# Kernel tuning notes

Hardware: AMD Instinct MI355X
Metric: run time of the kernel (lower is better)

## Reference

```python
import jax, jax.numpy as jnp
import numpy as np
from jax import lax

WIN = 11
SIGMA = 1.5
C1 = 0.01 ** 2
C2 = 0.03 ** 2


def _gauss_window(c):
    x = np.arange(WIN) - WIN // 2
    g = np.exp(-(x ** 2) / (2.0 * SIGMA ** 2))
    g = g / g.sum()
    w2d = np.outer(g, g).astype(np.float32)  # [11,11]
    return jnp.asarray(np.broadcast_to(w2d, (c, 1, WIN, WIN)).copy())


def _dwconv(x, kernel, groups):
    # x: [B,C,H,W], kernel: [C,1,kh,kw] depthwise, stride 1, SAME padding
    return lax.conv_general_dilated(
        x, kernel, window_strides=(1, 1), padding='SAME',
        dimension_numbers=('NCHW', 'OIHW', 'NCHW'),
        feature_group_count=groups)


_SOBEL_X = jnp.asarray(np.array([[-1, 0, 1], [-2, 0, 2], [-1, 0, 1]], np.float32))
_SOBEL_Y = jnp.asarray(np.array([[1, 2, 1], [0, 0, 0], [-1, -2, -1]], np.float32))


def _sobel_xy(x):
    # x: [B,3,H,W] -> depthwise 3x3 sobel on each channel (same as per-channel conv2d)
    c = x.shape[1]
    kx = jnp.broadcast_to(_SOBEL_X, (c, 1, 3, 3))
    ky = jnp.broadcast_to(_SOBEL_Y, (c, 1, 3, 3))
    return _dwconv(x, kx, c), _dwconv(x, ky, c)


def _rgb2ycrcb(im):
    R, G, B = im[:, 0:1], im[:, 1:2], im[:, 2:3]
    Y = 0.299 * R + 0.587 * G + 0.114 * B
    Cr = (R - Y) * 0.713 + 0.5
    Cb = (B - Y) * 0.564 + 0.5
    return Y, Cr, Cb


def _ssim(img1, img2, channel):
    w = _gauss_window(channel)
    mu1 = _dwconv(img1, w, channel)
    mu2 = _dwconv(img2, w, channel)
    mu1_sq = mu1 * mu1
    mu2_sq = mu2 * mu2
    mu12 = mu1 * mu2
    s1 = _dwconv(img1 * img1, w, channel) - mu1_sq
    s2 = _dwconv(img2 * img2, w, channel) - mu2_sq
    s12 = _dwconv(img1 * img2, w, channel) - mu12
    ssim_map = ((2 * mu12 + C1) * (2 * s12 + C2)) / ((mu1_sq + mu2_sq + C1) * (s1 + s2 + C2))
    return ssim_map.mean()


def _l1(a, b):
    return jnp.mean(jnp.abs(a - b))


def setup_inputs() -> dict:
    key = jax.random.key(0)
    k1, k2, k3 = jax.random.split(key, 3)
    shp = (16, 3, 512, 512)
    return {
        'input_vis': jax.random.uniform(k1, shp, jnp.float32),
        'input_ir': jax.random.uniform(k2, shp, jnp.float32),
        'fuse': jax.random.uniform(k3, shp, jnp.float32),
    }


def reference(input_vis, input_ir, fuse):
    # color components
    _, Cr_F, Cb_F = _rgb2ycrcb(fuse)
    _, Cr_V, Cb_V = _rgb2ycrcb(input_vis)
    Y_ir = input_ir[:, 0:1]

    # sobel gradients (depthwise over 3 channels == per-channel conv + cat)
    Fgx, Fgy = _sobel_xy(fuse)
    Vgx, Vgy = _sobel_xy(input_vis)
    Igx, Igy = _sobel_xy(input_ir)
    joint_gx = jnp.maximum(Vgx, Igx)
    joint_gy = jnp.maximum(Vgy, Igy)
    joint_int = jnp.maximum(input_vis, input_ir)

    con_loss = _l1(fuse, joint_int)
    gradient_loss = 0.5 * _l1(Fgx, joint_gx) + 0.5 * _l1(Fgy, joint_gy)
    color_loss = _l1(Cb_F, Cb_V) + _l1(Cr_F, Cr_V)

    # SSIM: rgb-vs-fused (3ch) and ir-Y vs gray(fused) (1ch)
    ssim_rgb = _ssim(input_vis, fuse, 3)
    gray_fused = (0.2989 * fuse[:, 0:1] + 0.587 * fuse[:, 1:2] + 0.114 * fuse[:, 2:3])
    ssim_ir = _ssim(Y_ir, gray_fused, 1)
    ssim_loss = 1.0 - (ssim_rgb + ssim_ir) / 2.0

    return 0.5 * con_loss + 0.2 * gradient_loss + 1.0 * color_loss + 0.1 * ssim_loss
```

## Files before the change

### kernel.cpp

```cpp
#include <hip/hip_runtime.h>

#define IMG_H 512
#define IMG_W 512
#define CH_STRIDE (IMG_H*IMG_W)
#define IMG_STRIDE (3*CH_STRIDE)

using f4    = __attribute__((ext_vector_type(4))) float;
using h4    = __attribute__((ext_vector_type(4))) _Float16;
using h8    = __attribute__((ext_vector_type(8))) _Float16;
using f32x4 = __attribute__((ext_vector_type(4))) float;

#define NSLOT 64
#define SLOT_F 32

__global__ __launch_bounds__(256) void k_zero(float* __restrict__ acc) {
  int i = threadIdx.x;
  *(f4*)&acc[i*8]     = f4{0,0,0,0};
  *(f4*)&acc[i*8 + 4] = f4{0,0,0,0};
}

__device__ __forceinline__ float block_sum(float v, float* red) {
  #pragma unroll
  for (int o = 32; o > 0; o >>= 1) v += __shfl_down(v, o, 64);
  __syncthreads();
  if ((threadIdx.x & 63) == 0) red[threadIdx.x >> 6] = v;
  __syncthreads();
  return red[0] + red[1] + red[2] + red[3];
}

#define R1W 68
#define R1N (18*R1W)

#define SXW 88
#define SXH 26
#define SF_STRIDE (SXH*SXW)
#define HB_OFF    (4*SF_STRIDE)
#define HB_F      (64*32)
#define WH_OFF    (HB_OFF + 4*HB_F)
#define WV_OFF    (WH_OFF + 512)
#define SMEM_H    (WV_OFF + 512)
#define SMEM_BYTES (SMEM_H*2)

#define N_SSIM 16384

__global__ __launch_bounds__(256, 4) void k_main(
    const float* __restrict__ vis, const float* __restrict__ ir,
    const float* __restrict__ fuse, float* __restrict__ acc)
{
  __shared__ __align__(16) char smem[SMEM_BYTES];
  __shared__ float red[4];
  const int tid = threadIdx.x;
  const int bid = blockIdx.x;
  float* aslot = acc + (bid & (NSLOT-1))*SLOT_F;

  if (bid < N_SSIM) {
    const int z = bid >> 8;
    const int n = z >> 2, pair = z & 3;
    const int x0 = (bid & 7)*64;
    const int y0 = ((bid >> 3) & 31)*16;
    _Float16* S = (_Float16*)smem;

    for (int i = tid; i < 1024; i += 256) {
      int m = i & 511;
      int col = m >> 5, k = m & 31;
      int j = (i < 512) ? (k - col - 3) : (k - col);
      float w = 0.f;
      if ((unsigned)j < 11u) {
        float d = (float)(j - 5);
        w = exp2f(-d*d*0.32059889798f) * 0.26601255681f;
      }
      S[(i < 512 ? WH_OFF : WV_OFF) + m] = (_Float16)w;
    }

    if (pair < 3) {
      const float* xb = vis  + (n*3 + pair)*CH_STRIDE;
      const float* yb = fuse + (n*3 + pair)*CH_STRIDE;
      for (int i = tid; i < SXH*20; i += 256) {
        int row = i / 20, k = i - row*20;
        int gy = y0 - 5 + row, gx = x0 - 8 + 4*k;
        f4 xv = {0,0,0,0}, yv = {0,0,0,0};
        if ((unsigned)gy < IMG_H && (unsigned)gx < IMG_W) {
          int off = gy*IMG_W + gx;
          xv = *(const f4*)&xb[off];
          yv = *(const f4*)&yb[off];
        }
        int ib = row*SXW + 4*k;
        h4 ax, by, pp, qq;
        #pragma unroll
        for (int j = 0; j < 4; ++j) {
          float xa = xv[j], ya = yv[j];
          ax[j] = (_Float16)xa;
          by[j] = (_Float16)ya;
          pp[j] = (_Float16)(xa*xa + ya*ya);
          qq[j] = (_Float16)(xa*ya);
        }
        *(h4*)&S[0*SF_STRIDE + ib] = ax;
        *(h4*)&S[1*SF_STRIDE + ib] = by;
        *(h4*)&S[2*SF_STRIDE + ib] = pp;
        *(h4*)&S[3*SF_STRIDE + ib] = qq;
      }
    } else {
      const float* xb = ir   + n*IMG_STRIDE;
      const float* fb = fuse + n*IMG_STRIDE;
      for (int i = tid; i < SXH*20; i += 256) {
        int row = i / 20, k = i - row*20;
        int gy = y0 - 5 + row, gx = x0 - 8 + 4*k;
        f4 xv = {0,0,0,0}, yv = {0,0,0,0};
        if ((unsigned)gy < IMG_H && (unsigned)gx < IMG_W) {
          int off = gy*IMG_W + gx;
          xv = *(const f4*)&xb[off];
          f4 rr = *(const f4*)&fb[off];
          f4 gg = *(const f4*)&fb[off + CH_STRIDE];
          f4 bb = *(const f4*)&fb[off + 2*CH_STRIDE];
          #pragma unroll
          for (int j = 0; j < 4; ++j)
            yv[j] = 0.2989f*rr[j] + 0.587f*gg[j] + 0.114f*bb[j];
        }
        int ib = row*SXW + 4*k;
        h4 ax, by, pp, qq;
        #pragma unroll
        for (int j = 0; j < 4; ++j) {
          float xa = xv[j], ya = yv[j];
          ax[j] = (_Float16)xa;
          by[j] = (_Float16)ya;
          pp[j] = (_Float16)(xa*xa + ya*ya);
          qq[j] = (_Float16)(xa*ya);
        }
        *(h4*)&S[0*SF_STRIDE + ib] = ax;
        *(h4*)&S[1*SF_STRIDE + ib] = by;
        *(h4*)&S[2*SF_STRIDE + ib] = pp;
        *(h4*)&S[3*SF_STRIDE + ib] = qq;
      }
    }
    __syncthreads();

    const int lr = tid & 15;
    const int lg = (tid >> 4) & 3;
    const int wv = tid >> 6;

    {
      h8 bh = *(const h8*)&S[WH_OFF + lr*32 + lg*8];
      const int xo = wv*16;
      #pragma unroll
      for (int rt = 0; rt < 2; ++rt) {
        int row_s = rt*16 + lr;
        int rcl = row_s > 25 ? 25 : row_s;
        bool zz = row_s > 25;
        #pragma unroll
        for (int f = 0; f < 4; ++f) {
          h8 a = *(const h8*)&S[f*SF_STRIDE + rcl*SXW + xo + lg*8];
          if (zz) a = h8{(_Float16)0,(_Float16)0,(_Float16)0,(_Float16)0,
                         (_Float16)0,(_Float16)0,(_Float16)0,(_Float16)0};
          f32x4 d = __builtin_amdgcn_mfma_f32_16x16x32_f16(
                        a, bh, f32x4{0.f,0.f,0.f,0.f}, 0, 0, 0);
          int px = xo + lr;
          int k0 = rt*16 + lg*4;
          h4 hv;
          #pragma unroll
          for (int r = 0; r < 4; ++r) hv[r] = (_Float16)d[r];
          int sgrp = (px ^ (px >> 2)) & 3;
          int b = k0 << 1;
          int sb = ((((b >> 4) ^ sgrp) << 4) | (b & 15));
          *(h4*)&S[HB_OFF + f*HB_F + px*32 + (sb >> 1)] = hv;
        }
      }
    }
    __syncthreads();

    float ss = 0.f;
    {
      h8 bv = *(const h8*)&S[WV_OFF + lr*32 + lg*8];
      const int pxA = wv*16 + lr;
      const int sgrp = (pxA ^ (pxA >> 2)) & 3;
      f32x4 dd[4];
      #pragma unroll
      for (int f = 0; f < 4; ++f) {
        int gi = lg ^ sgrp;
        h8 a = *(const h8*)&S[HB_OFF + f*HB_F + pxA*32 + gi*8];
        dd[f] = __builtin_amdgcn_mfma_f32_16x16x32_f16(
                    a, bv, f32x4{0.f,0.f,0.f,0.f}, 0, 0, 0);
      }
      #pragma unroll
      for (int r = 0; r < 4; ++r) {
        float mu1 = dd[0][r], mu2 = dd[1][r];
        float sP  = dd[2][r], sQ  = dd[3][r];
        float mu12 = mu1*mu2, mss = mu1*mu1 + mu2*mu2;
        float s12 = sQ - mu12, sps = sP - mss;
        ss += ((2.f*mu12 + 1e-4f)*(2.f*s12 + 9e-4f)) /
              ((mss + 1e-4f)*(sps + 9e-4f));
      }
    }
    float tot = block_sum(ss, red);
    if (tid == 0) atomicAdd(&aslot[(pair == 3) ? 6 : 5], tot);

  } else {
    const int r = bid - N_SSIM;
    const int x0 = (r & 7)*64;
    const int y0 = ((r >> 3) & 31)*16;
    const int n  = r >> 8;
    float* s = (float*)smem;
    const int ox = (tid & 15)*4;
    const int oy = tid >> 4;

    float con=0.f, gxs=0.f, gys=0.f, cbs=0.f, crs=0.f;
    float pv[3][4], pf[3][4];

    for (int c = 0; c < 3; ++c) {
      const float* pv0 = vis  + (n*3 + c)*CH_STRIDE;
      const float* pi0 = ir   + (n*3 + c)*CH_STRIDE;
      const float* pf0 = fuse + (n*3 + c)*CH_STRIDE;
      for (int i = tid; i < 864; i += 256) {
        int f = i / 288;
        int rr = i - f*288;
        int row = rr >> 4, k = rr & 15;
        int gy = y0 - 1 + row, gx = x0 + 4*k;
        f4 v = {0,0,0,0};
        const float* bp = (f == 0) ? pv0 : ((f == 1) ? pi0 : pf0);
        if ((unsigned)gy < IMG_H) v = *(const f4*)&bp[gy*IMG_W + gx];
        float* dst = s + f*R1N + row*R1W + 1 + 4*k;
        dst[0]=v.x; dst[1]=v.y; dst[2]=v.z; dst[3]=v.w;
      }
      if (tid < 108) {
        int f = tid / 36;
        int rr = tid - f*36;
        int row = rr >> 1, side = rr & 1;
        int gy = y0 - 1 + row;
        int gx = side ? (x0 + 64) : (x0 - 1);
        float v = 0.f;
        const float* bp = (f == 0) ? pv0 : ((f == 1) ? pi0 : pf0);
        if ((unsigned)gx < IMG_W && (unsigned)gy < IMG_H) v = bp[gy*IMG_W + gx];
        s[f*R1N + row*R1W + (side ? 65 : 0)] = v;
      }
      __syncthreads();

      float cen[3][4], gxv[3][4], gyv[3][4];
      #pragma unroll
      for (int t = 0; t < 3; ++t) {
        const float* sf = s + t*R1N;
        float r0[8], r1[8], r2[8];
        {
          f4 a = *(const f4*)&sf[(oy+0)*R1W + ox], b = *(const f4*)&sf[(oy+0)*R1W + ox + 4];
          r0[0]=a.x; r0[1]=a.y; r0[2]=a.z; r0[3]=a.w; r0[4]=b.x; r0[5]=b.y; r0[6]=b.z; r0[7]=b.w;
        }
        {
          f4 a = *(const f4*)&sf[(oy+1)*R1W + ox], b = *(const f4*)&sf[(oy+1)*R1W + ox + 4];
          r1[0]=a.x; r1[1]=a.y; r1[2]=a.z; r1[3]=a.w; r1[4]=b.x; r1[5]=b.y; r1[6]=b.z; r1[7]=b.w;
        }
        {
          f4 a = *(const f4*)&sf[(oy+2)*R1W + ox], b = *(const f4*)&sf[(oy+2)*R1W + ox + 4];
          r2[0]=a.x; r2[1]=a.y; r2[2]=a.z; r2[3]=a.w; r2[4]=b.x; r2[5]=b.y; r2[6]=b.z; r2[7]=b.w;
        }
        #pragma unroll
        for (int j = 0; j < 4; ++j) {
          gxv[t][j] = (r0[j+2]-r0[j]) + 2.f*(r1[j+2]-r1[j]) + (r2[j+2]-r2[j]);
          gyv[t][j] = (r0[j] + 2.f*r0[j+1] + r0[j+2]) - (r2[j] + 2.f*r2[j+1] + r2[j+2]);
          cen[t][j] = r1[j+1];
        }
      }
      #pragma unroll
      for (int j = 0; j < 4; ++j) {
        con += fabsf(cen[2][j] - fmaxf(cen[0][j], cen[1][j]));
        gxs += fabsf(gxv[2][j] - fmaxf(gxv[0][j], gxv[1][j]));
        gys += fabsf(gyv[2][j] - fmaxf(gyv[0][j], gyv[1][j]));
        pv[c][j] = cen[0][j];
        pf[c][j] = cen[2][j];
      }
      __syncthreads();
    }

    #pragma unroll
    for (int j = 0; j < 4; ++j) {
      float Yf = 0.299f*pf[0][j] + 0.587f*pf[1][j] + 0.114f*pf[2][j];
      float Yv = 0.299f*pv[0][j] + 0.587f*pv[1][j] + 0.114f*pv[2][j];
      crs += fabsf(0.713f*((pf[0][j]-Yf) - (pv[0][j]-Yv)));
      cbs += fabsf(0.564f*((pf[2][j]-Yf) - (pv[2][j]-Yv)));
    }

    float r0 = block_sum(con, red);
    float r1 = block_sum(gxs, red);
    float r2 = block_sum(gys, red);
    float r3 = block_sum(cbs, red);
    float r4 = block_sum(crs, red);
    if (tid == 0) {
      atomicAdd(&aslot[0], r0);
      atomicAdd(&aslot[1], r1);
      atomicAdd(&aslot[2], r2);
      atomicAdd(&aslot[3], r3);
      atomicAdd(&aslot[4], r4);
    }
  }
}

__global__ __launch_bounds__(64) void k_final(
    const float* __restrict__ acc, float* __restrict__ out)
{
  int lane = threadIdx.x;
  float s[7];
  #pragma unroll
  for (int c = 0; c < 7; ++c) {
    float x = acc[lane*SLOT_F + c];
    #pragma unroll
    for (int o = 32; o > 0; o >>= 1) x += __shfl_down(x, o, 64);
    s[c] = x;
  }
  if (lane == 0) {
    const float N3 = 16.f*3.f*512.f*512.f;
    const float N1 = 16.f*512.f*512.f;
    float con_loss  = s[0] / N3;
    float grad_loss = 0.5f*(s[1]/N3) + 0.5f*(s[2]/N3);
    float color_loss = s[3]/N1 + s[4]/N1;
    float ssim_loss = 1.f - (s[5]/N3 + s[6]/N1)*0.5f;
    out[0] = 0.5f*con_loss + 0.2f*grad_loss + color_loss + 0.1f*ssim_loss;
  }
}

extern "C" void kernel_launch(void* const* d_in, const int* in_sizes, int n_in,
                              void* d_out, int out_size, void* d_ws, size_t ws_size,
                              hipStream_t stream) {
  (void)in_sizes; (void)n_in; (void)out_size; (void)ws_size;
  const float* vis  = (const float*)d_in[0];
  const float* ir   = (const float*)d_in[1];
  const float* fuse = (const float*)d_in[2];
  float* out = (float*)d_out;
  float* acc = (float*)d_ws;

  k_zero<<<dim3(1,1,1), dim3(256,1,1), 0, stream>>>(acc);
  k_main<<<dim3(20480,1,1), dim3(256,1,1), 0, stream>>>(vis, ir, fuse, acc);
  k_final<<<dim3(1,1,1), dim3(64,1,1), 0, stream>>>(acc, out);
}
```

Measured before the change: 253.6 us.

## Shrink SSIM LDS footprint, compute weights in registers, interleave block types

The SSIM path now stores only the two fp16 input planes in LDS and forms the squared and cross products in registers before the horizontal MFMA. Gaussian weights are built directly in registers instead of staged through shared memory. This cuts LDS use so the launch bound can rise to 6 blocks per CU. The Sobel/L1 blocks are interleaved with the SSIM blocks (one per five) and read global memory directly instead of through LDS, with per-wave atomics replacing block reductions. In exchange there are more global loads and atomics, and the squares are now computed from fp16-rounded inputs, which changes precision.

After: 556.7 us. 120% more time.

```diff
diff --git a/kernel.cpp b/kernel.cpp
--- a/kernel.cpp
+++ b/kernel.cpp
@@ -19,57 +19,65 @@
   *(f4*)&acc[i*8 + 4] = f4{0,0,0,0};
 }
 
-__device__ __forceinline__ float block_sum(float v, float* red) {
-  #pragma unroll
-  for (int o = 32; o > 0; o >>= 1) v += __shfl_down(v, o, 64);
-  __syncthreads();
-  if ((threadIdx.x & 63) == 0) red[threadIdx.x >> 6] = v;
-  __syncthreads();
-  return red[0] + red[1] + red[2] + red[3];
-}
-
-#define R1W 68
-#define R1N (18*R1W)
-
-#define SXW 88
+__device__ __forceinline__ h4 cvt4(f4 v) {
+  return h4{(_Float16)v.x,(_Float16)v.y,(_Float16)v.z,(_Float16)v.w};
+}
+__device__ __forceinline__ h8 zero8() {
+  return h8{(_Float16)0,(_Float16)0,(_Float16)0,(_Float16)0,
+            (_Float16)0,(_Float16)0,(_Float16)0,(_Float16)0};
+}
+
+#define SXW 80
 #define SXH 26
 #define SF_STRIDE (SXH*SXW)
-#define HB_OFF    (4*SF_STRIDE)
+#define HB_OFF    (2*SF_STRIDE)
 #define HB_F      (64*32)
-#define WH_OFF    (HB_OFF + 4*HB_F)
-#define WV_OFF    (WH_OFF + 512)
-#define SMEM_H    (WV_OFF + 512)
-#define SMEM_BYTES (SMEM_H*2)
-
-#define N_SSIM 16384
-
-__global__ __launch_bounds__(256, 4) void k_main(
+#define SMEM_H    (HB_OFF + 4*HB_F)
+#define SMEM_BYTES (SMEM_H*2 + 128)
+
+__global__ __launch_bounds__(256, 6) void k_main(
     const float* __restrict__ vis, const float* __restrict__ ir,
     const float* __restrict__ fuse, float* __restrict__ acc)
 {
   __shared__ __align__(16) char smem[SMEM_BYTES];
-  __shared__ float red[4];
+  float* red = (float*)(smem + SMEM_H*2);
   const int tid = threadIdx.x;
   const int bid = blockIdx.x;
   float* aslot = acc + (bid & (NSLOT-1))*SLOT_F;
 
-  if (bid < N_SSIM) {
-    const int z = bid >> 8;
+  const int sb = bid / 5;
+  const int rm = bid - sb*5;
+
+  if (rm < 4) {
+    const int si = sb*4 + rm;
+    const int z = si >> 8;
     const int n = z >> 2, pair = z & 3;
-    const int x0 = (bid & 7)*64;
-    const int y0 = ((bid >> 3) & 31)*16;
+    const int x0 = (si & 7)*64;
+    const int y0 = ((si >> 3) & 31)*16;
     _Float16* S = (_Float16*)smem;
 
-    for (int i = tid; i < 1024; i += 256) {
-      int m = i & 511;
-      int col = m >> 5, k = m & 31;
-      int j = (i < 512) ? (k - col - 3) : (k - col);
-      float w = 0.f;
-      if ((unsigned)j < 11u) {
-        float d = (float)(j - 5);
-        w = exp2f(-d*d*0.32059889798f) * 0.26601255681f;
-      }
-      S[(i < 512 ? WH_OFF : WV_OFF) + m] = (_Float16)w;
+    const int lr = tid & 15;
+    const int lg = (tid >> 4) & 3;
+    const int wvw = tid >> 6;
+    const int xo = wvw*16;
+
+    h8 bh, bv;
+    #pragma unroll
+    for (int e = 0; e < 8; ++e) {
+      int k = lg*8 + e;
+      int jh = k - lr - 3;
+      int jv = k - lr;
+      float wh = 0.f, wvv = 0.f;
+      if ((unsigned)jh < 11u) {
+        float d = (float)(jh - 5);
+        wh = exp2f(-d*d*0.32059889798f) * 0.26601255681f;
+      }
+      if ((unsigned)jv < 11u) {
+        float d = (float)(jv - 5);
+        wvv = exp2f(-d*d*0.32059889798f) * 0.26601255681f;
+      }
+      bh[e] = (_Float16)wh;
+      bv[e] = (_Float16)wvv;
     }
 
     if (pair < 3) {
@@ -85,19 +93,8 @@
           yv = *(const f4*)&yb[off];
         }
         int ib = row*SXW + 4*k;
-        h4 ax, by, pp, qq;
-        #pragma unroll
-        for (int j = 0; j < 4; ++j) {
-          float xa = xv[j], ya = yv[j];
-          ax[j] = (_Float16)xa;
-          by[j] = (_Float16)ya;
-          pp[j] = (_Float16)(xa*xa + ya*ya);
-          qq[j] = (_Float16)(xa*ya);
-        }
-        *(h4*)&S[0*SF_STRIDE + ib] = ax;
-        *(h4*)&S[1*SF_STRIDE + ib] = by;
-        *(h4*)&S[2*SF_STRIDE + ib] = pp;
-        *(h4*)&S[3*SF_STRIDE + ib] = qq;
+        *(h4*)&S[ib]             = cvt4(xv);
+        *(h4*)&S[SF_STRIDE + ib] = cvt4(yv);
       }
     } else {
       const float* xb = ir   + n*IMG_STRIDE;
@@ -117,177 +114,168 @@
             yv[j] = 0.2989f*rr[j] + 0.587f*gg[j] + 0.114f*bb[j];
         }
         int ib = row*SXW + 4*k;
-        h4 ax, by, pp, qq;
-        #pragma unroll
-        for (int j = 0; j < 4; ++j) {
-          float xa = xv[j], ya = yv[j];
-          ax[j] = (_Float16)xa;
-          by[j] = (_Float16)ya;
-          pp[j] = (_Float16)(xa*xa + ya*ya);
-          qq[j] = (_Float16)(xa*ya);
-        }
-        *(h4*)&S[0*SF_STRIDE + ib] = ax;
-        *(h4*)&S[1*SF_STRIDE + ib] = by;
-        *(h4*)&S[2*SF_STRIDE + ib] = pp;
-        *(h4*)&S[3*SF_STRIDE + ib] = qq;
+        *(h4*)&S[ib]             = cvt4(xv);
+        *(h4*)&S[SF_STRIDE + ib] = cvt4(yv);
       }
     }
     __syncthreads();
 
-    const int lr = tid & 15;
-    const int lg = (tid >> 4) & 3;
-    const int wv = tid >> 6;
-
     {
-      h8 bh = *(const h8*)&S[WH_OFF + lr*32 + lg*8];
-      const int xo = wv*16;
+      const int px = xo + lr;
+      const int sgrp = (px ^ (px >> 2)) & 3;
       #pragma unroll
       for (int rt = 0; rt < 2; ++rt) {
         int row_s = rt*16 + lr;
         int rcl = row_s > 25 ? 25 : row_s;
-        bool zz = row_s > 25;
+        int rbase = rcl*SXW + xo + lg*8;
+        h8 a = *(const h8*)&S[rbase];
+        h8 b = *(const h8*)&S[SF_STRIDE + rbase];
+        if (row_s > 25) { a = zero8(); b = zero8(); }
+        h8 p = a*a + b*b;
+        h8 q = a*b;
+        f32x4 d0 = __builtin_amdgcn_mfma_f32_16x16x32_f16(
+                       a, bh, f32x4{0.f,0.f,0.f,0.f}, 0, 0, 0);
+        f32x4 d1 = __builtin_amdgcn_mfma_f32_16x16x32_f16(
+                       b, bh, f32x4{0.f,0.f,0.f,0.f}, 0, 0, 0);
+        f32x4 d2 = __builtin_amdgcn_mfma_f32_16x16x32_f16(
+                       p, bh, f32x4{0.f,0.f,0.f,0.f}, 0, 0, 0);
+        f32x4 d3 = __builtin_amdgcn_mfma_f32_16x16x32_f16(
+                       q, bh, f32x4{0.f,0.f,0.f,0.f}, 0, 0, 0);
+        int k0 = rt*16 + lg*4;
+        int bb2 = k0 << 1;
+        int sbk = ((((bb2 >> 4) ^ sgrp) << 4) | (bb2 & 15));
+        int base = HB_OFF + px*32 + (sbk >> 1);
+        h4 h0, h1, h2c, h3;
         #pragma unroll
-        for (int f = 0; f < 4; ++f) {
-          h8 a = *(const h8*)&S[f*SF_STRIDE + rcl*SXW + xo + lg*8];
-          if (zz) a = h8{(_Float16)0,(_Float16)0,(_Float16)0,(_Float16)0,
-                         (_Float16)0,(_Float16)0,(_Float16)0,(_Float16)0};
-          f32x4 d = __builtin_amdgcn_mfma_f32_16x16x32_f16(
-                        a, bh, f32x4{0.f,0.f,0.f,0.f}, 0, 0, 0);
-          int px = xo + lr;
-          int k0 = rt*16 + lg*4;
-          h4 hv;
-          #pragma unroll
-          for (int r = 0; r < 4; ++r) hv[r] = (_Float16)d[r];
-          int sgrp = (px ^ (px >> 2)) & 3;
-          int b = k0 << 1;
-          int sb = ((((b >> 4) ^ sgrp) << 4) | (b & 15));
-          *(h4*)&S[HB_OFF + f*HB_F + px*32 + (sb >> 1)] = hv;
-        }
+        for (int r2 = 0; r2 < 4; ++r2) {
+          h0[r2] = (_Float16)d0[r2];
+          h1[r2] = (_Float16)d1[r2];
+          h2c[r2] = (_Float16)d2[r2];
+          h3[r2] = (_Float16)d3[r2];
+        }
+        *(h4*)&S[base + 0*HB_F] = h0;
+        *(h4*)&S[base + 1*HB_F] = h1;
+        *(h4*)&S[base + 2*HB_F] = h2c;
+        *(h4*)&S[base + 3*HB_F] = h3;
       }
     }
     __syncthreads();
 
     float ss = 0.f;
     {
-      h8 bv = *(const h8*)&S[WV_OFF + lr*32 + lg*8];
-      const int pxA = wv*16 + lr;
+      const int pxA = xo + lr;
       const int sgrp = (pxA ^ (pxA >> 2)) & 3;
+      const int gi = lg ^ sgrp;
       f32x4 dd[4];
       #pragma unroll
       for (int f = 0; f < 4; ++f) {
-        int gi = lg ^ sgrp;
         h8 a = *(const h8*)&S[HB_OFF + f*HB_F + pxA*32 + gi*8];
         dd[f] = __builtin_amdgcn_mfma_f32_16x16x32_f16(
                     a, bv, f32x4{0.f,0.f,0.f,0.f}, 0, 0, 0);
       }
       #pragma unroll
-      for (int r = 0; r < 4; ++r) {
-        float mu1 = dd[0][r], mu2 = dd[1][r];
-        float sP  = dd[2][r], sQ  = dd[3][r];
+      for (int r2 = 0; r2 < 4; ++r2) {
+        float mu1 = dd[0][r2], mu2 = dd[1][r2];
+        float sP  = dd[2][r2], sQ  = dd[3][r2];
         float mu12 = mu1*mu2, mss = mu1*mu1 + mu2*mu2;
         float s12 = sQ - mu12, sps = sP - mss;
         ss += ((2.f*mu12 + 1e-4f)*(2.f*s12 + 9e-4f)) /
               ((mss + 1e-4f)*(sps + 9e-4f));
       }
     }
-    float tot = block_sum(ss, red);
-    if (tid == 0) atomicAdd(&aslot[(pair == 3) ? 6 : 5], tot);
+    #pragma unroll
+    for (int o = 32; o > 0; o >>= 1) ss += __shfl_down(ss, o, 64);
+    if ((tid & 63) == 0) atomicAdd(&aslot[(pair == 3) ? 6 : 5], ss);
 
   } else {
-    const int r = bid - N_SSIM;
+    const int r = sb;
     const int x0 = (r & 7)*64;
     const int y0 = ((r >> 3) & 31)*16;
     const int n  = r >> 8;
-    float* s = (float*)smem;
-    const int ox = (tid & 15)*4;
-    const int oy = tid >> 4;
+    const int gx = x0 + 4*(tid & 15);
+    const int gy = y0 + (tid >> 4);
 
     float con=0.f, gxs=0.f, gys=0.f, cbs=0.f, crs=0.f;
-    float pv[3][4], pf[3][4];
+    float pv0[4], pv2[4], pf0[4], pf2[4], Yv[4], Yf[4];
+    #pragma unroll
+    for (int j = 0; j < 4; ++j) { Yv[j]=0.f; Yf[j]=0.f; }
 
     for (int c = 0; c < 3; ++c) {
-      const float* pv0 = vis  + (n*3 + c)*CH_STRIDE;
-      const float* pi0 = ir   + (n*3 + c)*CH_STRIDE;
-      const float* pf0 = fuse + (n*3 + c)*CH_STRIDE;
-      for (int i = tid; i < 864; i += 256) {
-        int f = i / 288;
-        int rr = i - f*288;
-        int row = rr >> 4, k = rr & 15;
-        int gy = y0 - 1 + row, gx = x0 + 4*k;
-        f4 v = {0,0,0,0};
-        const float* bp = (f == 0) ? pv0 : ((f == 1) ? pi0 : pf0);
-        if ((unsigned)gy < IMG_H) v = *(const f4*)&bp[gy*IMG_W + gx];
-        float* dst = s + f*R1N + row*R1W + 1 + 4*k;
-        dst[0]=v.x; dst[1]=v.y; dst[2]=v.z; dst[3]=v.w;
-      }
-      if (tid < 108) {
-        int f = tid / 36;
-        int rr = tid - f*36;
-        int row = rr >> 1, side = rr & 1;
-        int gy = y0 - 1 + row;
-        int gx = side ? (x0 + 64) : (x0 - 1);
-        float v = 0.f;
-        const float* bp = (f == 0) ? pv0 : ((f == 1) ? pi0 : pf0);
-        if ((unsigned)gx < IMG_W && (unsigned)gy < IMG_H) v = bp[gy*IMG_W + gx];
-        s[f*R1N + row*R1W + (side ? 65 : 0)] = v;
-      }
-      __syncthreads();
-
-      float cen[3][4], gxv[3][4], gyv[3][4];
+      const float* bv_ = vis  + (n*3 + c)*CH_STRIDE;
+      const float* bi_ = ir   + (n*3 + c)*CH_STRIDE;
+      const float* bf_ = fuse + (n*3 + c)*CH_STRIDE;
+      const float yc = (c == 0) ? 0.299f : ((c == 1) ? 0.587f : 0.114f);
+      float mc[4], mx[4], my[4];
       #pragma unroll
       for (int t = 0; t < 3; ++t) {
-        const float* sf = s + t*R1N;
-        float r0[8], r1[8], r2[8];
-        {
-          f4 a = *(const f4*)&sf[(oy+0)*R1W + ox], b = *(const f4*)&sf[(oy+0)*R1W + ox + 4];
-          r0[0]=a.x; r0[1]=a.y; r0[2]=a.z; r0[3]=a.w; r0[4]=b.x; r0[5]=b.y; r0[6]=b.z; r0[7]=b.w;
-        }
-        {
-          f4 a = *(const f4*)&sf[(oy+1)*R1W + ox], b = *(const f4*)&sf[(oy+1)*R1W + ox + 4];
-          r1[0]=a.x; r1[1]=a.y; r1[2]=a.z; r1[3]=a.w; r1[4]=b.x; r1[5]=b.y; r1[6]=b.z; r1[7]=b.w;
-        }
-        {
-          f4 a = *(const f4*)&sf[(oy+2)*R1W + ox], b = *(const f4*)&sf[(oy+2)*R1W + ox + 4];
-          r2[0]=a.x; r2[1]=a.y; r2[2]=a.z; r2[3]=a.w; r2[4]=b.x; r2[5]=b.y; r2[6]=b.z; r2[7]=b.w;
-        }
+        const float* bp = (t == 0) ? bv_ : ((t == 1) ? bi_ : bf_);
+        float w[3][6];
+        #pragma unroll
+        for (int rr = 0; rr < 3; ++rr) {
+          int ry = gy - 1 + rr;
+          f4 m = {0,0,0,0}; float lft = 0.f, rgt = 0.f;
+          if ((unsigned)ry < IMG_H) {
+            const float* rp = bp + ry*IMG_W;
+            m = *(const f4*)&rp[gx];
+            if (gx > 0)   lft = rp[gx-1];
+            if (gx < 508) rgt = rp[gx+4];
+          }
+          w[rr][0]=lft; w[rr][1]=m.x; w[rr][2]=m.y; w[rr][3]=m.z;
+          w[rr][4]=m.w; w[rr][5]=rgt;
+        }
+        float cen[4], gxv[4], gyv[4];
         #pragma unroll
         for (int j = 0; j < 4; ++j) {
-          gxv[t][j] = (r0[j+2]-r0[j]) + 2.f*(r1[j+2]-r1[j]) + (r2[j+2]-r2[j]);
-          gyv[t][j] = (r0[j] + 2.f*r0[j+1] + r0[j+2]) - (r2[j] + 2.f*r2[j+1] + r2[j+2]);
-          cen[t][j] = r1[j+1];
-        }
-      }
-      #pragma unroll
-      for (int j = 0; j < 4; ++j) {
-        con += fabsf(cen[2][j] - fmaxf(cen[0][j], cen[1][j]));
-        gxs += fabsf(gxv[2][j] - fmaxf(gxv[0][j], gxv[1][j]));
-        gys += fabsf(gyv[2][j] - fmaxf(gyv[0][j], gyv[1][j]));
-        pv[c][j] = cen[0][j];
-        pf[c][j] = cen[2][j];
-      }
-      __syncthreads();
-    }
-
+          gxv[j] = (w[0][j+2]-w[0][j]) + 2.f*(w[1][j+2]-w[1][j]) + (w[2][j+2]-w[2][j]);
+          gyv[j] = (w[0][j] + 2.f*w[0][j+1] + w[0][j+2])
+                 - (w[2][j] + 2.f*w[2][j+1] + w[2][j+2]);
+          cen[j] = w[1][j+1];
+        }
+        if (t == 0) {
+          #pragma unroll
+          for (int j = 0; j < 4; ++j) {
+            mc[j]=cen[j]; mx[j]=gxv[j]; my[j]=gyv[j];
+            Yv[j] += yc*cen[j];
+            if (c == 0) pv0[j] = cen[j];
+            if (c == 2) pv2[j] = cen[j];
+          }
+        } else if (t == 1) {
+          #pragma unroll
+          for (int j = 0; j < 4; ++j) {
+            mc[j]=fmaxf(mc[j],cen[j]); mx[j]=fmaxf(mx[j],gxv[j]);
+            my[j]=fmaxf(my[j],gyv[j]);
+          }
+        } else {
+          #pragma unroll
+          for (int j = 0; j < 4; ++j) {
+            con += fabsf(cen[j] - mc[j]);
+            gxs += fabsf(gxv[j] - mx[j]);
+            gys += fabsf(gyv[j] - my[j]);
+            Yf[j] += yc*cen[j];
+            if (c == 0) pf0[j] = cen[j];
+            if (c == 2) pf2[j] = cen[j];
+          }
+        }
+      }
+    }
     #pragma unroll
     for (int j = 0; j < 4; ++j) {
-      float Yf = 0.299f*pf[0][j] + 0.587f*pf[1][j] + 0.114f*pf[2][j];
-      float Yv = 0.299f*pv[0][j] + 0.587f*pv[1][j] + 0.114f*pv[2][j];
-      crs += fabsf(0.713f*((pf[0][j]-Yf) - (pv[0][j]-Yv)));
-      cbs += fabsf(0.564f*((pf[2][j]-Yf) - (pv[2][j]-Yv)));
-    }
-
-    float r0 = block_sum(con, red);
-    float r1 = block_sum(gxs, red);
-    float r2 = block_sum(gys, red);
-    float r3 = block_sum(cbs, red);
-    float r4 = block_sum(crs, red);
-    if (tid == 0) {
-      atomicAdd(&aslot[0], r0);
-      atomicAdd(&aslot[1], r1);
-      atomicAdd(&aslot[2], r2);
-      atomicAdd(&aslot[3], r3);
-      atomicAdd(&aslot[4], r4);
-    }
+      crs += fabsf(0.713f*((pf0[j]-Yf[j]) - (pv0[j]-Yv[j])));
+      cbs += fabsf(0.564f*((pf2[j]-Yf[j]) - (pv2[j]-Yv[j])));
+    }
+
+    float sums[5] = {con, gxs, gys, cbs, crs};
+    const int lane = tid & 63, wvw = tid >> 6;
+    #pragma unroll
+    for (int i = 0; i < 5; ++i) {
+      float v = sums[i];
+      #pragma unroll
+      for (int o = 32; o > 0; o >>= 1) v += __shfl_down(v, o, 64);
+      if (lane == 0) red[wvw*5 + i] = v;
+    }
+    __syncthreads();
+    if (tid < 5)
+      atomicAdd(&aslot[tid], red[tid] + red[5+tid] + red[10+tid] + red[15+tid]);
   }
 }
 
```

## Process two SSIM row tiles per block with prefetch and on-the-fly products

Applied to the files above, without the earlier changes.

Each SSIM block now handles two 16-row tiles. Global loads for the second tile are issued before the first tile's horizontal MFMA pass and written to shared memory afterwards, so load latency overlaps compute. The squared and cross-product planes are formed in registers from the two staged fp16 inputs instead of being stored, which halves staging LDS. Gaussian weights are built in registers rather than shared memory, and the block reduction becomes per-wave atomics. The trade-offs are more registers, more atomics and fewer blocks, and squares are now taken of fp16-rounded inputs, which changes precision slightly.

Measured after the change: 236.1 us. 1.07x faster.

```diff
diff --git a/kernel.cpp b/kernel.cpp
--- a/kernel.cpp
+++ b/kernel.cpp
@@ -28,56 +28,153 @@
   return red[0] + red[1] + red[2] + red[3];
 }
 
+__device__ __forceinline__ h4 cvt4(f4 v) {
+  return h4{(_Float16)v.x,(_Float16)v.y,(_Float16)v.z,(_Float16)v.w};
+}
+__device__ __forceinline__ h8 zero8() {
+  return h8{(_Float16)0,(_Float16)0,(_Float16)0,(_Float16)0,
+            (_Float16)0,(_Float16)0,(_Float16)0,(_Float16)0};
+}
+
 #define R1W 68
 #define R1N (18*R1W)
 
 #define SXW 88
 #define SXH 26
 #define SF_STRIDE (SXH*SXW)
-#define HB_OFF    (4*SF_STRIDE)
+#define HB_OFF    (2*SF_STRIDE)
 #define HB_F      (64*32)
-#define WH_OFF    (HB_OFF + 4*HB_F)
-#define WV_OFF    (WH_OFF + 512)
-#define SMEM_H    (WV_OFF + 512)
-#define SMEM_BYTES (SMEM_H*2)
-
-#define N_SSIM 16384
+#define SMEM_H    (HB_OFF + 4*HB_F)
+#define SMEM_BYTES (SMEM_H*2 + 128)
+
+#define N_SSIM 8192
+
+__device__ __forceinline__ void phaseB(_Float16* S, h8 bh,
+                                       int lr, int lg, int xo) {
+  const int px = xo + lr;
+  const int sgrp = (px ^ (px >> 2)) & 3;
+  #pragma unroll
+  for (int rt = 0; rt < 2; ++rt) {
+    int row_s = rt*16 + lr;
+    int rcl = row_s > 25 ? 25 : row_s;
+    int rbase = rcl*SXW + xo + lg*8;
+    h8 a = *(const h8*)&S[rbase];
+    h8 b = *(const h8*)&S[SF_STRIDE + rbase];
+    if (row_s > 25) { a = zero8(); b = zero8(); }
+    h8 p = a*a + b*b;
+    h8 q = a*b;
+    f32x4 d0 = __builtin_amdgcn_mfma_f32_16x16x32_f16(
+                   a, bh, f32x4{0.f,0.f,0.f,0.f}, 0, 0, 0);
+    f32x4 d1 = __builtin_amdgcn_mfma_f32_16x16x32_f16(
+                   b, bh, f32x4{0.f,0.f,0.f,0.f}, 0, 0, 0);
+    f32x4 d2 = __builtin_amdgcn_mfma_f32_16x16x32_f16(
+                   p, bh, f32x4{0.f,0.f,0.f,0.f}, 0, 0, 0);
+    f32x4 d3 = __builtin_amdgcn_mfma_f32_16x16x32_f16(
+                   q, bh, f32x4{0.f,0.f,0.f,0.f}, 0, 0, 0);
+    int k0 = rt*16 + lg*4;
+    int bb2 = k0 << 1;
+    int sbk = ((((bb2 >> 4) ^ sgrp) << 4) | (bb2 & 15));
+    int base = HB_OFF + px*32 + (sbk >> 1);
+    h4 h0, h1, h2c, h3;
+    #pragma unroll
+    for (int r2 = 0; r2 < 4; ++r2) {
+      h0[r2]  = (_Float16)d0[r2];
+      h1[r2]  = (_Float16)d1[r2];
+      h2c[r2] = (_Float16)d2[r2];
+      h3[r2]  = (_Float16)d3[r2];
+    }
+    *(h4*)&S[base + 0*HB_F] = h0;
+    *(h4*)&S[base + 1*HB_F] = h1;
+    *(h4*)&S[base + 2*HB_F] = h2c;
+    *(h4*)&S[base + 3*HB_F] = h3;
+  }
+}
+
+__device__ __forceinline__ float phaseC(const _Float16* S, h8 bv,
+                                        int lr, int lg, int xo) {
+  const int pxA = xo + lr;
+  const int sgrp = (pxA ^ (pxA >> 2)) & 3;
+  const int gi = lg ^ sgrp;
+  f32x4 dd[4];
+  #pragma unroll
+  for (int f = 0; f < 4; ++f) {
+    h8 a = *(const h8*)&S[HB_OFF + f*HB_F + pxA*32 + gi*8];
+    dd[f] = __builtin_amdgcn_mfma_f32_16x16x32_f16(
+                a, bv, f32x4{0.f,0.f,0.f,0.f}, 0, 0, 0);
+  }
+  float ss = 0.f;
+  #pragma unroll
+  for (int r2 = 0; r2 < 4; ++r2) {
+    float mu1 = dd[0][r2], mu2 = dd[1][r2];
+    float sP  = dd[2][r2], sQ  = dd[3][r2];
+    float mu12 = mu1*mu2, mss = mu1*mu1 + mu2*mu2;
+    float s12 = sQ - mu12, sps = sP - mss;
+    ss += ((2.f*mu12 + 1e-4f)*(2.f*s12 + 9e-4f)) /
+          ((mss + 1e-4f)*(sps + 9e-4f));
+  }
+  return ss;
+}
 
 __global__ __launch_bounds__(256, 4) void k_main(
     const float* __restrict__ vis, const float* __restrict__ ir,
     const float* __restrict__ fuse, float* __restrict__ acc)
 {
   __shared__ __align__(16) char smem[SMEM_BYTES];
-  __shared__ float red[4];
+  float* red = (float*)(smem + SMEM_H*2);
   const int tid = threadIdx.x;
   const int bid = blockIdx.x;
   float* aslot = acc + (bid & (NSLOT-1))*SLOT_F;
 
   if (bid < N_SSIM) {
-    const int z = bid >> 8;
+    const int z = bid >> 7;
     const int n = z >> 2, pair = z & 3;
     const int x0 = (bid & 7)*64;
-    const int y0 = ((bid >> 3) & 31)*16;
+    const int y0a = ((bid >> 3) & 15)*32;
+    const int y0b = y0a + 16;
     _Float16* S = (_Float16*)smem;
 
-    for (int i = tid; i < 1024; i += 256) {
-      int m = i & 511;
-      int col = m >> 5, k = m & 31;
-      int j = (i < 512) ? (k - col - 3) : (k - col);
-      float w = 0.f;
-      if ((unsigned)j < 11u) {
-        float d = (float)(j - 5);
-        w = exp2f(-d*d*0.32059889798f) * 0.26601255681f;
-      }
-      S[(i < 512 ? WH_OFF : WV_OFF) + m] = (_Float16)w;
-    }
-
+    const int lr = tid & 15;
+    const int lg = (tid >> 4) & 3;
+    const int wvw = tid >> 6;
+    const int xo = wvw*16;
+
+    const float* xb;
+    const float* yb;
     if (pair < 3) {
-      const float* xb = vis  + (n*3 + pair)*CH_STRIDE;
-      const float* yb = fuse + (n*3 + pair)*CH_STRIDE;
+      xb = vis  + (n*3 + pair)*CH_STRIDE;
+      yb = fuse + (n*3 + pair)*CH_STRIDE;
+    } else {
+      xb = ir   + n*IMG_STRIDE;
+      yb = fuse + n*IMG_STRIDE;
+    }
+
+    h8 bh, bv;
+    #pragma unroll
+    for (int e = 0; e < 8; ++e) {
+      int k = lg*8 + e;
+      int jh = k - lr - 3;
+      int jv = k - lr;
+      float wh = 0.f, wvv = 0.f;
+      if ((unsigned)jh < 11u) {
+        float d = (float)(jh - 5);
+        wh = exp2f(-d*d*0.32059889798f) * 0.26601255681f;
+      }
+      if ((unsigned)jv < 11u) {
+        float d = (float)(jv - 5);
+        wvv = exp2f(-d*d*0.32059889798f) * 0.26601255681f;
+      }
+      bh[e] = (_Float16)wh;
+      bv[e] = (_Float16)wvv;
+    }
+
+    const int row0 = tid / 20,        k0c = tid - row0*20;
+    const int i1r  = tid + 256;
+    const int row1 = i1r / 20,        k1c = i1r - row1*20;
+
+    if (pair < 3) {
       for (int i = tid; i < SXH*20; i += 256) {
         int row = i / 20, k = i - row*20;
-        int gy = y0 - 5 + row, gx = x0 - 8 + 4*k;
+        int gy = y0a - 5 + row, gx = x0 - 8 + 4*k;
         f4 xv = {0,0,0,0}, yv = {0,0,0,0};
         if ((unsigned)gy < IMG_H && (unsigned)gx < IMG_W) {
           int off = gy*IMG_W + gx;
@@ -85,113 +182,113 @@
           yv = *(const f4*)&yb[off];
         }
         int ib = row*SXW + 4*k;
-        h4 ax, by, pp, qq;
-        #pragma unroll
-        for (int j = 0; j < 4; ++j) {
-          float xa = xv[j], ya = yv[j];
-          ax[j] = (_Float16)xa;
-          by[j] = (_Float16)ya;
-          pp[j] = (_Float16)(xa*xa + ya*ya);
-          qq[j] = (_Float16)(xa*ya);
-        }
-        *(h4*)&S[0*SF_STRIDE + ib] = ax;
-        *(h4*)&S[1*SF_STRIDE + ib] = by;
-        *(h4*)&S[2*SF_STRIDE + ib] = pp;
-        *(h4*)&S[3*SF_STRIDE + ib] = qq;
+        *(h4*)&S[ib]             = cvt4(xv);
+        *(h4*)&S[SF_STRIDE + ib] = cvt4(yv);
       }
     } else {
-      const float* xb = ir   + n*IMG_STRIDE;
-      const float* fb = fuse + n*IMG_STRIDE;
       for (int i = tid; i < SXH*20; i += 256) {
         int row = i / 20, k = i - row*20;
-        int gy = y0 - 5 + row, gx = x0 - 8 + 4*k;
+        int gy = y0a - 5 + row, gx = x0 - 8 + 4*k;
         f4 xv = {0,0,0,0}, yv = {0,0,0,0};
         if ((unsigned)gy < IMG_H && (unsigned)gx < IMG_W) {
           int off = gy*IMG_W + gx;
           xv = *(const f4*)&xb[off];
-          f4 rr = *(const f4*)&fb[off];
-          f4 gg = *(const f4*)&fb[off + CH_STRIDE];
-          f4 bb = *(const f4*)&fb[off + 2*CH_STRIDE];
+          f4 rr = *(const f4*)&yb[off];
+          f4 gg = *(const f4*)&yb[off + CH_STRIDE];
+          f4 bb = *(const f4*)&yb[off + 2*CH_STRIDE];
           #pragma unroll
           for (int j = 0; j < 4; ++j)
             yv[j] = 0.2989f*rr[j] + 0.587f*gg[j] + 0.114f*bb[j];
         }
         int ib = row*SXW + 4*k;
-        h4 ax, by, pp, qq;
+        *(h4*)&S[ib]             = cvt4(xv);
+        *(h4*)&S[SF_STRIDE + ib] = cvt4(yv);
+      }
+    }
+    __syncthreads();
+
+    f4 p0x = {0,0,0,0}, p0y = {0,0,0,0}, p1x = {0,0,0,0}, p1y = {0,0,0,0};
+    f4 q0g = {0,0,0,0}, q0b = {0,0,0,0}, q1g = {0,0,0,0}, q1b = {0,0,0,0};
+    {
+      int gy0 = y0b - 5 + row0, gx0 = x0 - 8 + 4*k0c;
+      int gy1 = y0b - 5 + row1, gx1 = x0 - 8 + 4*k1c;
+      bool v0 = (unsigned)gy0 < IMG_H && (unsigned)gx0 < IMG_W;
+      bool v1 = (unsigned)gy1 < IMG_H && (unsigned)gx1 < IMG_W;
+      int o0 = gy0*IMG_W + gx0, o1 = gy1*IMG_W + gx1;
+      if (pair < 3) {
+        if (v0) { p0x = *(const f4*)&xb[o0]; p0y = *(const f4*)&yb[o0]; }
+        if (v1) { p1x = *(const f4*)&xb[o1]; p1y = *(const f4*)&yb[o1]; }
+      } else {
+        if (v0) {
+          p0x = *(const f4*)&xb[o0];
+          p0y = *(const f4*)&yb[o0];
+          q0g = *(const f4*)&yb[o0 + CH_STRIDE];
+          q0b = *(const f4*)&yb[o0 + 2*CH_STRIDE];
+        }
+        if (v1) {
+          p1x = *(const f4*)&xb[o1];
+          p1y = *(const f4*)&yb[o1];
+          q1g = *(const f4*)&yb[o1 + CH_STRIDE];
+          q1b = *(const f4*)&yb[o1 + 2*CH_STRIDE];
+        }
+      }
+    }
+
+    phaseB(S, bh, lr, lg, xo);
+    __syncthreads();
+
+    {
+      int ib0 = row0*SXW + 4*k0c;
+      int ib1 = row1*SXW + 4*k1c;
+      if (pair < 3) {
+        *(h4*)&S[ib0]             = cvt4(p0x);
+        *(h4*)&S[SF_STRIDE + ib0] = cvt4(p0y);
+        *(h4*)&S[ib1]             = cvt4(p1x);
+        *(h4*)&S[SF_STRIDE + ib1] = cvt4(p1y);
+      } else {
+        f4 l0, l1;
         #pragma unroll
         for (int j = 0; j < 4; ++j) {
-          float xa = xv[j], ya = yv[j];
-          ax[j] = (_Float16)xa;
-          by[j] = (_Float16)ya;
-          pp[j] = (_Float16)(xa*xa + ya*ya);
-          qq[j] = (_Float16)(xa*ya);
-        }
-        *(h4*)&S[0*SF_STRIDE + ib] = ax;
-        *(h4*)&S[1*SF_STRIDE + ib] = by;
-        *(h4*)&S[2*SF_STRIDE + ib] = pp;
-        *(h4*)&S[3*SF_STRIDE + ib] = qq;
-      }
-    }
+          l0[j] = 0.2989f*p0y[j] + 0.587f*q0g[j] + 0.114f*q0b[j];
+          l1[j] = 0.2989f*p1y[j] + 0.587f*q1g[j] + 0.114f*q1b[j];
+        }
+        *(h4*)&S[ib0]             = cvt4(p0x);
+        *(h4*)&S[SF_STRIDE + ib0] = cvt4(l0);
+        *(h4*)&S[ib1]             = cvt4(p1x);
+        *(h4*)&S[SF_STRIDE + ib1] = cvt4(l1);
+      }
+      if (tid < 8) {
+        int k2 = tid + 12;
+        int gy2 = y0b + 20, gx2 = x0 - 8 + 4*k2;
+        f4 xv = {0,0,0,0}, yv = {0,0,0,0};
+        if ((unsigned)gy2 < IMG_H && (unsigned)gx2 < IMG_W) {
+          int off = gy2*IMG_W + gx2;
+          xv = *(const f4*)&xb[off];
+          if (pair < 3) yv = *(const f4*)&yb[off];
+          else {
+            f4 rr = *(const f4*)&yb[off];
+            f4 gg = *(const f4*)&yb[off + CH_STRIDE];
+            f4 bb = *(const f4*)&yb[off + 2*CH_STRIDE];
+            #pragma unroll
+            for (int j = 0; j < 4; ++j)
+              yv[j] = 0.2989f*rr[j] + 0.587f*gg[j] + 0.114f*bb[j];
+          }
+        }
+        int ib2 = 25*SXW + 4*k2;
+        *(h4*)&S[ib2]             = cvt4(xv);
+        *(h4*)&S[SF_STRIDE + ib2] = cvt4(yv);
+      }
+    }
+
+    float ss = phaseC(S, bv, lr, lg, xo);
     __syncthreads();
-
-    const int lr = tid & 15;
-    const int lg = (tid >> 4) & 3;
-    const int wv = tid >> 6;
-
-    {
-      h8 bh = *(const h8*)&S[WH_OFF + lr*32 + lg*8];
-      const int xo = wv*16;
-      #pragma unroll
-      for (int rt = 0; rt < 2; ++rt) {
-        int row_s = rt*16 + lr;
-        int rcl = row_s > 25 ? 25 : row_s;
-        bool zz = row_s > 25;
-        #pragma unroll
-        for (int f = 0; f < 4; ++f) {
-          h8 a = *(const h8*)&S[f*SF_STRIDE + rcl*SXW + xo + lg*8];
-          if (zz) a = h8{(_Float16)0,(_Float16)0,(_Float16)0,(_Float16)0,
-                         (_Float16)0,(_Float16)0,(_Float16)0,(_Float16)0};
-          f32x4 d = __builtin_amdgcn_mfma_f32_16x16x32_f16(
-                        a, bh, f32x4{0.f,0.f,0.f,0.f}, 0, 0, 0);
-          int px = xo + lr;
-          int k0 = rt*16 + lg*4;
-          h4 hv;
-          #pragma unroll
-          for (int r = 0; r < 4; ++r) hv[r] = (_Float16)d[r];
-          int sgrp = (px ^ (px >> 2)) & 3;
-          int b = k0 << 1;
-          int sb = ((((b >> 4) ^ sgrp) << 4) | (b & 15));
-          *(h4*)&S[HB_OFF + f*HB_F + px*32 + (sb >> 1)] = hv;
-        }
-      }
-    }
+    phaseB(S, bh, lr, lg, xo);
     __syncthreads();
-
-    float ss = 0.f;
-    {
-      h8 bv = *(const h8*)&S[WV_OFF + lr*32 + lg*8];
-      const int pxA = wv*16 + lr;
-      const int sgrp = (pxA ^ (pxA >> 2)) & 3;
-      f32x4 dd[4];
-      #pragma unroll
-      for (int f = 0; f < 4; ++f) {
-        int gi = lg ^ sgrp;
-        h8 a = *(const h8*)&S[HB_OFF + f*HB_F + pxA*32 + gi*8];
-        dd[f] = __builtin_amdgcn_mfma_f32_16x16x32_f16(
-                    a, bv, f32x4{0.f,0.f,0.f,0.f}, 0, 0, 0);
-      }
-      #pragma unroll
-      for (int r = 0; r < 4; ++r) {
-        float mu1 = dd[0][r], mu2 = dd[1][r];
-        float sP  = dd[2][r], sQ  = dd[3][r];
-        float mu12 = mu1*mu2, mss = mu1*mu1 + mu2*mu2;
-        float s12 = sQ - mu12, sps = sP - mss;
-        ss += ((2.f*mu12 + 1e-4f)*(2.f*s12 + 9e-4f)) /
-              ((mss + 1e-4f)*(sps + 9e-4f));
-      }
-    }
-    float tot = block_sum(ss, red);
-    if (tid == 0) atomicAdd(&aslot[(pair == 3) ? 6 : 5], tot);
+    ss += phaseC(S, bv, lr, lg, xo);
+
+    #pragma unroll
+    for (int o = 32; o > 0; o >>= 1) ss += __shfl_down(ss, o, 64);
+    if ((tid & 63) == 0) atomicAdd(&aslot[(pair == 3) ? 6 : 5], ss);
 
   } else {
     const int r = bid - N_SSIM;
@@ -325,6 +422,6 @@
   float* acc = (float*)d_ws;
 
   k_zero<<<dim3(1,1,1), dim3(256,1,1), 0, stream>>>(acc);
-  k_main<<<dim3(20480,1,1), dim3(256,1,1), 0, stream>>>(vis, ir, fuse, acc);
+  k_main<<<dim3(12288,1,1), dim3(256,1,1), 0, stream>>>(vis, ir, fuse, acc);
   k_final<<<dim3(1,1,1), dim3(64,1,1), 0, stream>>>(acc, out);
 }
```
